# Kernel tuning notes

Hardware: AMD Instinct MI355X
Metric: run time of the kernel (lower is better)

Reference implementation:

```python
import jax, jax.numpy as jnp
import numpy as np

LEVEL = 3
NUM_BANDS = LEVEL + 1
B, N, D_MODEL, PATCH_NUMS, PRED_LEN = 32, 7, 768, 64, 336

# db4 lowpass decomposition filter (pywt convention)
_DB4_DEC_LO = np.array([
    -0.010597401784997278, 0.032883011666982945, 0.030841381835986965,
    -0.18703481171888114, -0.02798376941698385, 0.6308807679295904,
    0.7148465705525415, 0.23037781330885523], dtype=np.float32)
REC_LO = _DB4_DEC_LO[::-1].copy()                                   # reconstruction lowpass
REC_HI = (_DB4_DEC_LO * ((-1.0) ** (np.arange(8) + 1))).astype(np.float32)  # reconstruction highpass (QMF)


def _upsample2(x):
    # zero-interleave along last axis: (..., L) -> (..., 2L)
    z = jnp.zeros_like(x)
    return jnp.stack([x, z], axis=-1).reshape(*x.shape[:-1], 2 * x.shape[-1])


def _idwt_per(ca, cd, rec_lo, rec_hi):
    # single-level inverse DWT, periodization mode, along last axis: (..., L) -> (..., 2L)
    F = rec_lo.shape[0]
    ua, ud = _upsample2(ca), _upsample2(cd)
    y = jnp.zeros_like(ua)
    for k in range(F):  # small fixed tap loop (F=8)
        y = y + jnp.roll(ua, k, axis=-1) * rec_lo[k] + jnp.roll(ud, k, axis=-1) * rec_hi[k]
    return jnp.roll(y, -(F // 2 - 1), axis=-1)  # compensate filter delay


def _iswt(coeffs, level, rec_lo, rec_hi):
    # coeffs: (..., T, level+1) with bands ordered [cA, cD_level, ..., cD1]
    T = coeffs.shape[-2]
    out = coeffs[..., 0]
    for j in range(level, 0, -1):
        step = 2 ** (j - 1)
        cd = coeffs[..., level - j + 1]
        M = T // step
        # gather the `step` interleaved subsequences as a batch axis: (..., step, M)
        o = jnp.moveaxis(out.reshape(*out.shape[:-1], M, step), -1, -2)
        d = jnp.moveaxis(cd.reshape(*cd.shape[:-1], M, step), -1, -2)
        x1 = _idwt_per(o[..., 0::2], d[..., 0::2], rec_lo, rec_hi)
        x2 = jnp.roll(_idwt_per(o[..., 1::2], d[..., 1::2], rec_lo, rec_hi), 1, axis=-1)
        new = 0.5 * (x1 + x2)  # (..., step, M)
        out = jnp.moveaxis(new, -2, -1).reshape(*out.shape[:-1], T)
    return out


def setup_inputs() -> dict:
    key = jax.random.key(0)
    kx, kw, kb = jax.random.split(key, 3)
    Din = D_MODEL * PATCH_NUMS
    x = jax.random.normal(kx, (B, N, D_MODEL, PATCH_NUMS), dtype=jnp.float32)
    # Linear init ~ U(-1/sqrt(Din), 1/sqrt(Din)); small normal is equivalent for a reference
    W = jax.random.normal(kw, (NUM_BANDS, Din, PRED_LEN), dtype=jnp.float32) * (1.0 / np.sqrt(Din))
    b = jax.random.normal(kb, (NUM_BANDS, PRED_LEN), dtype=jnp.float32) * 0.01
    return {"x": x, "W": W, "b": b}


def reference(x, W, b):
    # x: (B, N, d_model, patch_nums); W: (bands, d_model*patch_nums, pred_len); b: (bands, pred_len)
    Bb, Nn, dm, P = x.shape
    xf = x.reshape(Bb, Nn, dm * P)  # Flatten(start_dim=-2)
    # all band projections as one batched GEMM -> (B, N, pred_len, bands)
    coeffs = jnp.einsum('bnd,kdp->bnpk', xf, W) + b.T
    rec_lo = jnp.asarray(REC_LO)
    rec_hi = jnp.asarray(REC_HI)
    return _iswt(coeffs, LEVEL, rec_lo, rec_hi)  # (B, N, pred_len)
```

## Files before the change

### kernel.cpp

```cpp
#include <hip/hip_runtime.h>
#include <stdint.h>

#define M_ROWS   224
#define K_DIM    49152
#define NCOL     1344
#define PRED     336
#define S_CHUNKS 48
#define STEPS    32

#define XB_OFFSET (32u * 1024u * 1024u)

typedef __attribute__((ext_vector_type(8))) short short8;
typedef __attribute__((ext_vector_type(4))) float floatx4;

__device__ __forceinline__ uint16_t f32_to_bf16(float f) {
    uint32_t u = __builtin_bit_cast(uint32_t, f);
    uint32_t r = (u + 0x7fffu + ((u >> 16) & 1u)) >> 16;
    return (uint16_t)r;
}
__device__ __forceinline__ float bf16_to_f32(uint16_t h) {
    uint32_t u = ((uint32_t)h) << 16;
    return __builtin_bit_cast(float, u);
}
__device__ __forceinline__ uint32_t pack2(float lo, float hi) {
    return (uint32_t)f32_to_bf16(lo) | ((uint32_t)f32_to_bf16(hi) << 16);
}

__global__ __launch_bounds__(256) void cvt_x(
    const float* __restrict__ X, uint16_t* __restrict__ Xb)
{
    const size_t i = ((size_t)blockIdx.x * 256 + threadIdx.x) * 8;
    const float4 a = *(const float4*)(X + i);
    const float4 b = *(const float4*)(X + i + 4);
    uint4 o;
    o.x = pack2(a.x, a.y);
    o.y = pack2(a.z, a.w);
    o.z = pack2(b.x, b.y);
    o.w = pack2(b.z, b.w);
    *(uint4*)(Xb + i) = o;
}

__global__ __launch_bounds__(256, 4) void gemm_partial(
    const uint16_t* __restrict__ Xb,
    const float* __restrict__ W,
    uint16_t* __restrict__ P)
{
    __shared__ uint16_t lA[2][14 * 512];

    const int id = blockIdx.x;
    const int g  = id & 7;
    const int q  = id >> 3;
    const int ct = q % 21;
    const int s  = g + 8 * (q / 21);

    const int tid  = threadIdx.x;
    const int lane = tid & 63;
    const int w    = tid >> 6;
    const int l15  = lane & 15;
    const int kq   = lane >> 4;
    const int c0w  = ct * 64 + w * 16;
    const int band = c0w / PRED;
    const int p0   = c0w - band * PRED;

    const float* wbase = W + (size_t)band * ((size_t)K_DIM * PRED)
                           + (size_t)(kq * 8) * PRED
                           + (size_t)(p0 + l15);
    const size_t grow = (size_t)l15 * K_DIM + (size_t)kq * 8;
    const int kbase = s * (STEPS * 32);

    floatx4 acc[14];
    #pragma unroll
    for (int f = 0; f < 14; ++f) acc[f] = (floatx4){0.f, 0.f, 0.f, 0.f};

    float wcur[8], wnxt[8];

    #pragma unroll
    for (int j = 0; j < 8; ++j) wcur[j] = wbase[(size_t)(kbase + j) * PRED];
    #pragma unroll
    for (int t = 0; t < 4; ++t) {
        const int f = w + 4 * t;
        if (f < 14) {
            const uint16_t* gp = Xb + (size_t)(16 * f) * K_DIM + grow + kbase;
            __builtin_amdgcn_global_load_lds(
                (const __attribute__((address_space(1))) void*)gp,
                (__attribute__((address_space(3))) void*)&lA[0][f * 512],
                16, 0, 0);
        }
    }

    for (int st = 0; st < STEPS; ++st) {
        __syncthreads();
        const int cur = st & 1;

        if (st + 1 < STEPS) {
            const int kn = kbase + (st + 1) * 32;
            #pragma unroll
            for (int t = 0; t < 4; ++t) {
                const int f = w + 4 * t;
                if (f < 14) {
                    const uint16_t* gp = Xb + (size_t)(16 * f) * K_DIM + grow + kn;
                    __builtin_amdgcn_global_load_lds(
                        (const __attribute__((address_space(1))) void*)gp,
                        (__attribute__((address_space(3))) void*)&lA[cur ^ 1][f * 512],
                        16, 0, 0);
                }
            }
            #pragma unroll
            for (int j = 0; j < 8; ++j) wnxt[j] = wbase[(size_t)(kn + j) * PRED];
        }

        short8 bfrag;
        #pragma unroll
        for (int j = 0; j < 4; ++j)
            ((uint32_t*)&bfrag)[j] = pack2(wcur[2 * j], wcur[2 * j + 1]);

        #pragma unroll
        for (int f = 0; f < 14; ++f) {
            short8 afrag = *(const short8*)&lA[cur][f * 512 + lane * 8];
            acc[f] = __builtin_amdgcn_mfma_f32_16x16x32_bf16(afrag, bfrag, acc[f], 0, 0, 0);
        }

        if (st + 1 < STEPS) {
            #pragma unroll
            for (int j = 0; j < 8; ++j) wcur[j] = wnxt[j];
        }
    }

    const int col = c0w + l15;
    #pragma unroll
    for (int f = 0; f < 14; ++f) {
        #pragma unroll
        for (int r = 0; r < 4; ++r) {
            const int m = 16 * f + kq * 4 + r;
            P[((size_t)m * S_CHUNKS + s) * NCOL + col] = f32_to_bf16(acc[f][r]);
        }
    }
}

__device__ const float REC_LO[8] = {
     0.23037781330885523f,  0.7148465705525415f,   0.6308807679295904f,
    -0.02798376941698385f, -0.18703481171888114f,  0.030841381835986965f,
     0.032883011666982945f, -0.010597401784997278f };
__device__ const float REC_HI[8] = {
     0.010597401784997278f, 0.032883011666982945f, -0.030841381835986965f,
    -0.18703481171888114f,  0.02798376941698385f,   0.6308807679295904f,
    -0.7148465705525415f,   0.23037781330885523f };

__global__ __launch_bounds__(1024) void reduce_iswt(
    const uint16_t* __restrict__ P,
    const float* __restrict__ bias,
    float* __restrict__ out)
{
    __shared__ float coeff[NCOL];
    __shared__ float buf[2][PRED];

    const int row = blockIdx.x;
    const int tid = threadIdx.x;
    const uint32_t* pr = (const uint32_t*)(P + (size_t)row * S_CHUNKS * NCOL);

    if (tid < NCOL / 2) {
        float a0 = 0.f, a1 = 0.f;
        #pragma unroll 4
        for (int s = 0; s < S_CHUNKS; ++s) {
            const uint32_t v = pr[s * (NCOL / 2) + tid];
            a0 += bf16_to_f32((uint16_t)(v & 0xffff));
            a1 += bf16_to_f32((uint16_t)(v >> 16));
        }
        coeff[2 * tid]     = a0 + bias[2 * tid];
        coeff[2 * tid + 1] = a1 + bias[2 * tid + 1];
    }
    __syncthreads();

    if (tid < PRED) buf[0][tid] = coeff[tid];
    __syncthreads();

    int curb = 0;
    for (int j = 3; j >= 1; --j) {
        const int step = 1 << (j - 1);
        const int M    = PRED / step;
        const float* cd  = &coeff[(4 - j) * PRED];
        const float* cur = buf[curb];
        float* nxt       = buf[curb ^ 1];
        if (tid < PRED) {
            const int t = tid;
            const int sidx = t & (step - 1);
            const int m = t / step;
            const int mm1 = (m == 0) ? (M - 1) : (m - 1);
            float x1 = 0.f, x2 = 0.f;
            #pragma unroll
            for (int k = 0; k < 8; ++k) {
                int i1 = m + 3 - k;  if (i1 < 0) i1 += M; else if (i1 >= M) i1 -= M;
                if ((i1 & 1) == 0) {
                    const int pos = i1 * step + sidx;
                    x1 += cur[pos] * REC_LO[k] + cd[pos] * REC_HI[k];
                }
                int i2 = mm1 + 3 - k;  if (i2 < 0) i2 += M; else if (i2 >= M) i2 -= M;
                if ((i2 & 1) == 0) {
                    const int pos = (i2 + 1) * step + sidx;
                    x2 += cur[pos] * REC_LO[k] + cd[pos] * REC_HI[k];
                }
            }
            nxt[t] = 0.5f * (x1 + x2);
        }
        __syncthreads();
        curb ^= 1;
    }

    if (tid < PRED) out[(size_t)row * PRED + tid] = buf[curb][tid];
}

extern "C" void kernel_launch(void* const* d_in, const int* in_sizes, int n_in,
                              void* d_out, int out_size, void* d_ws, size_t ws_size,
                              hipStream_t stream) {
    const float* X    = (const float*)d_in[0];
    const float* W    = (const float*)d_in[1];
    const float* bias = (const float*)d_in[2];
    float* out        = (float*)d_out;
    uint16_t* P       = (uint16_t*)d_ws;
    uint16_t* Xb      = (uint16_t*)((char*)d_ws + XB_OFFSET);

    cvt_x       <<<5376, 256, 0, stream>>>(X, Xb);
    gemm_partial<<<21 * S_CHUNKS, 256, 0, stream>>>(Xb, W, P);
    reduce_iswt <<<M_ROWS, 1024, 0, stream>>>(P, bias, out);
}
```

Before: 428.8 us.

## Fuse X bf16 conversion into GEMM loads and halve split-K chunks

Drops the separate cvt_x kernel. The GEMM now loads fp32 X into registers, packs it to bf16 and writes it into LDS itself, instead of using direct global-to-LDS loads of pre-converted data. The split-K factor goes from 48 to 24 chunks with twice the steps per chunk, and the occupancy hint is lowered to 2 blocks per CU. This removes a kernel launch and a full write and re-read of the bf16 X buffer, and shrinks the partial buffer. In exchange it reads fp32 X, which is twice the bytes, once per column tile (21 tiles), launches half as many blocks, and adds VALU packing work inside the loop.

```diff
diff --git a/kernel.cpp b/kernel.cpp
--- a/kernel.cpp
+++ b/kernel.cpp
@@ -5,10 +5,9 @@
 #define K_DIM    49152
 #define NCOL     1344
 #define PRED     336
-#define S_CHUNKS 48
-#define STEPS    32
-
-#define XB_OFFSET (32u * 1024u * 1024u)
+#define S_CHUNKS 24
+#define STEPS    64
+
 
 typedef __attribute__((ext_vector_type(8))) short short8;
 typedef __attribute__((ext_vector_type(4))) float floatx4;
@@ -26,22 +25,8 @@
     return (uint32_t)f32_to_bf16(lo) | ((uint32_t)f32_to_bf16(hi) << 16);
 }
 
-__global__ __launch_bounds__(256) void cvt_x(
-    const float* __restrict__ X, uint16_t* __restrict__ Xb)
-{
-    const size_t i = ((size_t)blockIdx.x * 256 + threadIdx.x) * 8;
-    const float4 a = *(const float4*)(X + i);
-    const float4 b = *(const float4*)(X + i + 4);
-    uint4 o;
-    o.x = pack2(a.x, a.y);
-    o.y = pack2(a.z, a.w);
-    o.z = pack2(b.x, b.y);
-    o.w = pack2(b.z, b.w);
-    *(uint4*)(Xb + i) = o;
-}
-
-__global__ __launch_bounds__(256, 4) void gemm_partial(
-    const uint16_t* __restrict__ Xb,
+__global__ __launch_bounds__(256, 2) void gemm_partial(
+    const float* __restrict__ X,
     const float* __restrict__ W,
     uint16_t* __restrict__ P)
 {
@@ -65,7 +50,7 @@
     const float* wbase = W + (size_t)band * ((size_t)K_DIM * PRED)
                            + (size_t)(kq * 8) * PRED
                            + (size_t)(p0 + l15);
-    const size_t grow = (size_t)l15 * K_DIM + (size_t)kq * 8;
+    const float* xbase = X + (size_t)l15 * K_DIM + (size_t)(kq * 8);
     const int kbase = s * (STEPS * 32);
 
     floatx4 acc[14];
@@ -73,18 +58,29 @@
     for (int f = 0; f < 14; ++f) acc[f] = (floatx4){0.f, 0.f, 0.f, 0.f};
 
     float wcur[8], wnxt[8];
-
-    #pragma unroll
-    for (int j = 0; j < 8; ++j) wcur[j] = wbase[(size_t)(kbase + j) * PRED];
+    float4 xr[4][2];
+
     #pragma unroll
     for (int t = 0; t < 4; ++t) {
         const int f = w + 4 * t;
         if (f < 14) {
-            const uint16_t* gp = Xb + (size_t)(16 * f) * K_DIM + grow + kbase;
-            __builtin_amdgcn_global_load_lds(
-                (const __attribute__((address_space(1))) void*)gp,
-                (__attribute__((address_space(3))) void*)&lA[0][f * 512],
-                16, 0, 0);
+            const float* gp = xbase + (size_t)(16 * f) * K_DIM + kbase;
+            xr[t][0] = *(const float4*)gp;
+            xr[t][1] = *(const float4*)(gp + 4);
+        }
+    }
+    #pragma unroll
+    for (int j = 0; j < 8; ++j) wcur[j] = wbase[(size_t)(kbase + j) * PRED];
+    #pragma unroll
+    for (int t = 0; t < 4; ++t) {
+        const int f = w + 4 * t;
+        if (f < 14) {
+            short8 v;
+            ((uint32_t*)&v)[0] = pack2(xr[t][0].x, xr[t][0].y);
+            ((uint32_t*)&v)[1] = pack2(xr[t][0].z, xr[t][0].w);
+            ((uint32_t*)&v)[2] = pack2(xr[t][1].x, xr[t][1].y);
+            ((uint32_t*)&v)[3] = pack2(xr[t][1].z, xr[t][1].w);
+            *(short8*)&lA[0][f * 512 + lane * 8] = v;
         }
     }
 
@@ -98,11 +94,9 @@
             for (int t = 0; t < 4; ++t) {
                 const int f = w + 4 * t;
                 if (f < 14) {
-                    const uint16_t* gp = Xb + (size_t)(16 * f) * K_DIM + grow + kn;
-                    __builtin_amdgcn_global_load_lds(
-                        (const __attribute__((address_space(1))) void*)gp,
-                        (__attribute__((address_space(3))) void*)&lA[cur ^ 1][f * 512],
-                        16, 0, 0);
+                    const float* gp = xbase + (size_t)(16 * f) * K_DIM + kn;
+                    xr[t][0] = *(const float4*)gp;
+                    xr[t][1] = *(const float4*)(gp + 4);
                 }
             }
             #pragma unroll
@@ -121,6 +115,18 @@
         }
 
         if (st + 1 < STEPS) {
+            #pragma unroll
+            for (int t = 0; t < 4; ++t) {
+                const int f = w + 4 * t;
+                if (f < 14) {
+                    short8 v;
+                    ((uint32_t*)&v)[0] = pack2(xr[t][0].x, xr[t][0].y);
+                    ((uint32_t*)&v)[1] = pack2(xr[t][0].z, xr[t][0].w);
+                    ((uint32_t*)&v)[2] = pack2(xr[t][1].x, xr[t][1].y);
+                    ((uint32_t*)&v)[3] = pack2(xr[t][1].z, xr[t][1].w);
+                    *(short8*)&lA[cur ^ 1][f * 512 + lane * 8] = v;
+                }
+            }
             #pragma unroll
             for (int j = 0; j < 8; ++j) wcur[j] = wnxt[j];
         }
@@ -160,7 +166,7 @@
 
     if (tid < NCOL / 2) {
         float a0 = 0.f, a1 = 0.f;
-        #pragma unroll 4
+        #pragma unroll 8
         for (int s = 0; s < S_CHUNKS; ++s) {
             const uint32_t v = pr[s * (NCOL / 2) + tid];
             a0 += bf16_to_f32((uint16_t)(v & 0xffff));
@@ -217,9 +223,7 @@
     const float* bias = (const float*)d_in[2];
     float* out        = (float*)d_out;
     uint16_t* P       = (uint16_t*)d_ws;
-    uint16_t* Xb      = (uint16_t*)((char*)d_ws + XB_OFFSET);
-
-    cvt_x       <<<5376, 256, 0, stream>>>(X, Xb);
-    gemm_partial<<<21 * S_CHUNKS, 256, 0, stream>>>(Xb, W, P);
+
+    gemm_partial<<<21 * S_CHUNKS, 256, 0, stream>>>(X, W, P);
     reduce_iswt <<<M_ROWS, 1024, 0, stream>>>(P, bias, out);
 }
```

New measurement: 518.0 us. +20.8%, slower.

## Load A fragments directly from global memory instead of LDS double-buffering

Applied to the files above, without the earlier changes.

The GEMM kernel drops the shared-memory double buffer for X tiles and has each wave read its bf16 A fragments straight from global memory, relying on the 4x loop unroll to keep loads in flight. It also removes the per-step block barrier, lowers the occupancy hint in launch_bounds from 4 to 2 to allow more registers, and raises the unroll factor of the reduce loop. The risk is that all four waves now fetch the same A data redundantly through L1/L2 instead of sharing one LDS copy, and explicit prefetching of W is gone.

```diff
diff --git a/kernel.cpp b/kernel.cpp
--- a/kernel.cpp
+++ b/kernel.cpp
@@ -40,13 +40,11 @@
     *(uint4*)(Xb + i) = o;
 }
 
-__global__ __launch_bounds__(256, 4) void gemm_partial(
+__global__ __launch_bounds__(256, 2) void gemm_partial(
     const uint16_t* __restrict__ Xb,
     const float* __restrict__ W,
     uint16_t* __restrict__ P)
 {
-    __shared__ uint16_t lA[2][14 * 512];
-
     const int id = blockIdx.x;
     const int g  = id & 7;
     const int q  = id >> 3;
@@ -61,68 +59,36 @@
     const int c0w  = ct * 64 + w * 16;
     const int band = c0w / PRED;
     const int p0   = c0w - band * PRED;
+    const int kbase = s * (STEPS * 32);
 
-    const float* wbase = W + (size_t)band * ((size_t)K_DIM * PRED)
-                           + (size_t)(kq * 8) * PRED
-                           + (size_t)(p0 + l15);
-    const size_t grow = (size_t)l15 * K_DIM + (size_t)kq * 8;
-    const int kbase = s * (STEPS * 32);
+    const uint16_t* abase = Xb + (size_t)l15 * K_DIM + (size_t)(kq * 8) + kbase;
+    const float* wlane = W + (size_t)band * ((size_t)K_DIM * PRED)
+                           + (size_t)(kq * 8) * PRED + (size_t)(p0 + l15);
 
     floatx4 acc[14];
     #pragma unroll
     for (int f = 0; f < 14; ++f) acc[f] = (floatx4){0.f, 0.f, 0.f, 0.f};
 
-    float wcur[8], wnxt[8];
+    #pragma unroll 4
+    for (int st = 0; st < STEPS; ++st) {
+        const int k0 = st * 32;
 
-    #pragma unroll
-    for (int j = 0; j < 8; ++j) wcur[j] = wbase[(size_t)(kbase + j) * PRED];
-    #pragma unroll
-    for (int t = 0; t < 4; ++t) {
-        const int f = w + 4 * t;
-        if (f < 14) {
-            const uint16_t* gp = Xb + (size_t)(16 * f) * K_DIM + grow + kbase;
-            __builtin_amdgcn_global_load_lds(
-                (const __attribute__((address_space(1))) void*)gp,
-                (__attribute__((address_space(3))) void*)&lA[0][f * 512],
-                16, 0, 0);
-        }
-    }
-
-    for (int st = 0; st < STEPS; ++st) {
-        __syncthreads();
-        const int cur = st & 1;
-
-        if (st + 1 < STEPS) {
-            const int kn = kbase + (st + 1) * 32;
-            #pragma unroll
-            for (int t = 0; t < 4; ++t) {
-                const int f = w + 4 * t;
-                if (f < 14) {
-                    const uint16_t* gp = Xb + (size_t)(16 * f) * K_DIM + grow + kn;
-                    __builtin_amdgcn_global_load_lds(
-                        (const __attribute__((address_space(1))) void*)gp,
-                        (__attribute__((address_space(3))) void*)&lA[cur ^ 1][f * 512],
-                        16, 0, 0);
-                }
-            }
-            #pragma unroll
-            for (int j = 0; j < 8; ++j) wnxt[j] = wbase[(size_t)(kn + j) * PRED];
-        }
+        float wv[8];
+        #pragma unroll
+        for (int j = 0; j < 8; ++j)
+            wv[j] = wlane[(size_t)(kbase + k0 + j) * PRED];
 
         short8 bfrag;
         #pragma unroll
         for (int j = 0; j < 4; ++j)
-            ((uint32_t*)&bfrag)[j] = pack2(wcur[2 * j], wcur[2 * j + 1]);
+            ((uint32_t*)&bfrag)[j] = pack2(wv[2 * j], wv[2 * j + 1]);
 
         #pragma unroll
         for (int f = 0; f < 14; ++f) {
-            short8 afrag = *(const short8*)&lA[cur][f * 512 + lane * 8];
-            acc[f] = __builtin_amdgcn_mfma_f32_16x16x32_bf16(afrag, bfrag, acc[f], 0, 0, 0);
-        }
-
-        if (st + 1 < STEPS) {
-            #pragma unroll
-            for (int j = 0; j < 8; ++j) wcur[j] = wnxt[j];
+            const short8 afrag =
+                *(const short8*)(abase + (size_t)(16 * f) * K_DIM + k0);
+            acc[f] = __builtin_amdgcn_mfma_f32_16x16x32_bf16(
+                afrag, bfrag, acc[f], 0, 0, 0);
         }
     }
 
@@ -160,7 +126,7 @@
 
     if (tid < NCOL / 2) {
         float a0 = 0.f, a1 = 0.f;
-        #pragma unroll 4
+        #pragma unroll 8
         for (int s = 0; s < S_CHUNKS; ++s) {
             const uint32_t v = pr[s * (NCOL / 2) + tid];
             a0 += bf16_to_f32((uint16_t)(v & 0xffff));
```

New measurement: 744.6 us. +73.6%, slower.
